# Optimization experiments

Measured on AMD Instinct MI355X. Metric: run time of the kernel, lower is better.

Reference implementation:

```python
import jax, jax.numpy as jnp
from jax import lax
import numpy as np

B, L, V = 8192, 64, 10000


def setup_inputs() -> dict:
    key = jax.random.key(0)
    k1, k2, k3, k4 = jax.random.split(key, 4)
    tokens1 = jax.random.randint(k1, (B, L), 0, V, dtype=jnp.int32)
    tokens2 = jax.random.randint(k2, (B, L), 0, V, dtype=jnp.int32)
    len1 = jax.random.randint(k3, (B,), 0, L, dtype=jnp.int32)
    len2 = jax.random.randint(k4, (B,), 0, L, dtype=jnp.int32)
    sub_cost = jnp.ones((1,), dtype=jnp.float32)
    return {"tokens1": tokens1, "tokens2": tokens2, "len1": len1,
            "len2": len2, "sub_cost": sub_cost}


def _edit_one(a, b, la, lb, c):
    # a, b: [L] int32 token ids; la, lb: scalar lengths; c: substitution cost
    Lp = a.shape[0]
    row0 = jnp.arange(Lp + 1, dtype=jnp.float32)  # D[0, :] = j

    def outer(prev, ai):
        # compute row i of the Levenshtein DP table from row i-1
        first = prev[0] + 1.0  # D[i, 0] = i

        def inner(left, xs):
            p_jm1, p_j, bj = xs  # D[i-1,j-1], D[i-1,j], b[j-1]
            cost = jnp.where(ai == bj, 0.0, c)
            v = jnp.minimum(jnp.minimum(p_j + 1.0, left + 1.0), p_jm1 + cost)
            return v, v

        _, tail = lax.scan(inner, first, (prev[:-1], prev[1:], b))
        new_row = jnp.concatenate([first[None], tail])  # [L+1]
        return new_row, new_row

    _, rows = lax.scan(outer, row0, a)              # [L, L+1]
    table = jnp.concatenate([row0[None], rows], 0)  # [L+1, L+1]
    # edit distance of the length-la prefix of a vs length-lb prefix of b
    return table[la, lb]


def reference(tokens1, tokens2, len1, len2, sub_cost):
    c = sub_cost[0]
    dist = jax.vmap(lambda a, b, la, lb: _edit_one(a, b, la, lb, c))(
        tokens1, tokens2, len1, len2)  # [B]
    return dist.reshape(-1, 1)  # matches tf.reshape(dist, [-1, 1])
```

## Files before the change

kernel.cpp:

```cpp
#include <hip/hip_runtime.h>

#define WAVE 64

__device__ __forceinline__ int rf(int x) { return __builtin_amdgcn_readfirstlane(x); }
__device__ __forceinline__ float bperm_f(int addr, float v) {
    return __int_as_float(__builtin_amdgcn_ds_bpermute(addr, __float_as_int(v)));
}
__device__ __forceinline__ int bperm_i(int addr, int v) {
    return __builtin_amdgcn_ds_bpermute(addr, v);
}

__global__ __launch_bounds__(256) void edit_distance_kernel(
    const int* __restrict__ t1, const int* __restrict__ t2,
    const int* __restrict__ len1, const int* __restrict__ len2,
    const float* __restrict__ subc, float* __restrict__ out, int B)
{
    const int tid  = blockIdx.x * blockDim.x + threadIdx.x;
    const int pair = tid >> 6;
    const int lane = tid & (WAVE - 1);
    if (pair >= B) return;

    const float c      = subc[0];
    const int   a_tok  = t1[pair * 64 + lane];
    const int   b_tok  = t2[pair * 64 + lane];
    const int   la     = rf(len1[pair]);
    const int   lb     = rf(len2[pair]);
    const bool  unit_c = (rf(__float_as_int(c)) == __float_as_int(1.0f));

    if (unit_c) {
        const bool sw  = lb > la;
        const int  m   = sw ? lb : la;
        const int  n   = sw ? la : lb;
        const int  pat = sw ? b_tok : a_tok;
        const int  txt = sw ? a_tok : b_tok;

        const int pat_m = (lane < m) ? pat : -2;
        const int txt_m = (lane < n) ? txt : -1;

        unsigned long long any = 0ull;
#pragma unroll
        for (int j = 0; j < 64; ++j) {
            const int bj = __builtin_amdgcn_readlane(txt_m, j);
            any |= __ballot(pat_m == bj);
        }

        if (any == 0ull) {
            if (lane == 0) out[pair] = (float)m;
            return;
        }

        unsigned long long Pv = ~0ull, Mv = 0ull;
        for (int j = 0; j < n; ++j) {
            const int bj = __builtin_amdgcn_readlane(txt, j);
            const unsigned long long Eq = __ballot(pat_m == bj);
            if ((Eq | Mv) == 0ull) {
                Pv <<= 1;
            } else {
                const unsigned long long Xv = Eq | Mv;
                const unsigned long long Xh = (((Eq & Pv) + Pv) ^ Pv) | Eq;
                unsigned long long Ph = Mv | ~(Xh | Pv);
                const unsigned long long Mh = Pv & Xh;
                Ph = (Ph << 1) | 1ull;
                Pv = (Mh << 1) | ~(Xv | Ph);
                Mv = Ph & Xv;
            }
        }
        const unsigned long long mask = ~0ull >> (64 - m);
        const int score = n + __popcll(Pv & mask) - __popcll(Mv & mask);
        if (lane == 0) out[pair] = (float)score;
    } else {
        const int rotaddr = ((lane + 63) & 63) << 2;
        int bcur = bperm_i(((64 - lane) & 63) << 2, b_tok);
        const int  tmax   = rf(la + lb - 1);
        const bool lane0  = (lane == 0);
        const int  target = lb + lane - 1;

        float cur   = (float)(lane + 1);
        float diagn = 0.f;
        float saved = 0.f;
        float ft    = 0.f;

        for (int t = 0; t < tmax; ++t) {
            float up   = bperm_f(rotaddr, cur);
            float diag = diagn;
            if (lane0) { up = ft + 1.f; diag = ft; }

            const float cost = (a_tok == bcur) ? 0.f : c;
            const float v = fminf(fminf(up, cur) + 1.f, diag + cost);

            if (t >= lane) {
                cur = v;
                if (t == target) saved = v;
            }
            diagn = up;
            bcur  = bperm_i(rotaddr, bcur);
            ft   += 1.f;
        }

        int src = (la > 0) ? (la - 1) : 0;
        float ans = __shfl(saved, src, WAVE);
        if (la == 0)      ans = (float)lb;
        else if (lb == 0) ans = (float)la;

        if (lane == 0) out[pair] = ans;
    }
}

extern "C" void kernel_launch(void* const* d_in, const int* in_sizes, int n_in,
                              void* d_out, int out_size, void* d_ws, size_t ws_size,
                              hipStream_t stream) {
    const int*   tokens1 = (const int*)d_in[0];
    const int*   tokens2 = (const int*)d_in[1];
    const int*   len1    = (const int*)d_in[2];
    const int*   len2    = (const int*)d_in[3];
    const float* subc    = (const float*)d_in[4];
    float*       out     = (float*)d_out;

    const int B = in_sizes[2];
    const int threads = 256;
    const int blocks  = (B * WAVE + threads - 1) / threads;
    edit_distance_kernel<<<blocks, threads, 0, stream>>>(
        tokens1, tokens2, len1, len2, subc, out, B);
}
```

Baseline: 70.40 us.

## Skip non-matching columns in bit-parallel Myers loop using a match column mask

The match pre-check now loops only over the actual text length n rather than all 64 lanes, and it records a per-column bitmask of which text positions have any match. The Myers bit-vector loop then visits only matching columns. Runs of non-matching columns use a cheaper Eq=0 update while Mv is nonzero, and a single bulk shift of Pv once Mv is zero. This cuts the readlane/ballot work and loop iterations on random, sparsely matching tokens. In exchange it adds data-dependent control flow, and the pre-check loop is no longer fully unrolled.

```diff
diff --git a/kernel.cpp b/kernel.cpp
--- a/kernel.cpp
+++ b/kernel.cpp
@@ -33,38 +33,54 @@
         const int  n   = sw ? la : lb;
         const int  pat = sw ? b_tok : a_tok;
         const int  txt = sw ? a_tok : b_tok;
+        const int  pat_m = (lane < m) ? pat : -2;
 
-        const int pat_m = (lane < m) ? pat : -2;
-        const int txt_m = (lane < n) ? txt : -1;
-
-        unsigned long long any = 0ull;
-#pragma unroll
-        for (int j = 0; j < 64; ++j) {
-            const int bj = __builtin_amdgcn_readlane(txt_m, j);
-            any |= __ballot(pat_m == bj);
+        unsigned long long colmask = 0ull;
+        for (int j = 0; j < n; ++j) {
+            const int bj = __builtin_amdgcn_readlane(txt, j);
+            const unsigned long long Eq = __ballot(pat_m == bj);
+            colmask |= (unsigned long long)(Eq != 0ull) << j;
         }
 
-        if (any == 0ull) {
+        if (colmask == 0ull) {
             if (lane == 0) out[pair] = (float)m;
             return;
         }
 
         unsigned long long Pv = ~0ull, Mv = 0ull;
-        for (int j = 0; j < n; ++j) {
-            const int bj = __builtin_amdgcn_readlane(txt, j);
+        unsigned long long cols = colmask;
+        int jcur = 0;
+        while (cols) {
+            const int jn = __builtin_ctzll(cols);
+            cols &= cols - 1;
+            while (jcur < jn && Mv != 0ull) {
+                unsigned long long Ph = ((Mv | ~Pv) << 1) | 1ull;
+                const unsigned long long Pv2 = ~(Mv | Ph);
+                Mv = Ph & Mv;
+                Pv = Pv2;
+                ++jcur;
+            }
+            if (jcur < jn) { Pv <<= (jn - jcur); jcur = jn; }
+            const int bj = __builtin_amdgcn_readlane(txt, jn);
             const unsigned long long Eq = __ballot(pat_m == bj);
-            if ((Eq | Mv) == 0ull) {
-                Pv <<= 1;
-            } else {
-                const unsigned long long Xv = Eq | Mv;
-                const unsigned long long Xh = (((Eq & Pv) + Pv) ^ Pv) | Eq;
-                unsigned long long Ph = Mv | ~(Xh | Pv);
-                const unsigned long long Mh = Pv & Xh;
-                Ph = (Ph << 1) | 1ull;
-                Pv = (Mh << 1) | ~(Xv | Ph);
-                Mv = Ph & Xv;
-            }
+            const unsigned long long Xv = Eq | Mv;
+            const unsigned long long Xh = (((Eq & Pv) + Pv) ^ Pv) | Eq;
+            unsigned long long Ph = Mv | ~(Xh | Pv);
+            const unsigned long long Mh = Pv & Xh;
+            Ph = (Ph << 1) | 1ull;
+            Pv = (Mh << 1) | ~(Xv | Ph);
+            Mv = Ph & Xv;
+            jcur = jn + 1;
         }
+        while (Mv != 0ull && jcur < n) {
+            unsigned long long Ph = ((Mv | ~Pv) << 1) | 1ull;
+            const unsigned long long Pv2 = ~(Mv | Ph);
+            Mv = Ph & Mv;
+            Pv = Pv2;
+            ++jcur;
+        }
+        Pv <<= (n - jcur);
+
         const unsigned long long mask = ~0ull >> (64 - m);
         const int score = n + __popcll(Pv & mask) - __popcll(Mv & mask);
         if (lane == 0) out[pair] = (float)score;
```

Measured after the change: 68.60 us. 2.6% less time.
